# Performance work log

Hardware: AMD Instinct MI355X
Metric: run time of the kernel (lower is better)

The kernel has to match this reference:

```python
import jax, jax.numpy as jnp
import numpy as np


def _conv3d(x, w, b, strides):
    # x: (N, C, D, H, W), w: (O, I, kD, kH, kW), VALID padding like torch Conv3d p=0
    y = jax.lax.conv_general_dilated(
        x, w, window_strides=strides, padding='VALID',
        dimension_numbers=('NCDHW', 'OIDHW', 'NCDHW'))
    return y + b.reshape(1, -1, 1, 1, 1)


def _avgpool3d(x, k):
    y = jax.lax.reduce_window(x, 0.0, jax.lax.add,
                              (1, 1, k, k, k), (1, 1, k, k, k), 'VALID')
    return y / float(k ** 3)


def setup_inputs() -> dict:
    key = jax.random.key(0)
    ks = jax.random.split(key, 11)
    f = jnp.float32
    return {
        'x':  jax.random.normal(ks[0], (1, 10, 1, 52, 7, 24), dtype=f),
        'w1': jax.random.normal(ks[1], (1, 1, 6, 2, 2), dtype=f) * 0.2,
        'b1': jax.random.normal(ks[2], (1,), dtype=f) * 0.1,
        'w2': jax.random.normal(ks[3], (1, 1, 4, 1, 2), dtype=f) * 0.2,
        'b2': jax.random.normal(ks[4], (1,), dtype=f) * 0.1,
        'w4': jax.random.normal(ks[5], (80, 27), dtype=f) * 0.19,
        'b4': jax.random.normal(ks[6], (80,), dtype=f) * 0.1,
        'w5': jax.random.normal(ks[7], (200, 80), dtype=f) * 0.11,
        'b5': jax.random.normal(ks[8], (200,), dtype=f) * 0.1,
        'w6': jax.random.normal(ks[9], (676, 200), dtype=f) * 0.07,
        'b6': jax.random.normal(ks[10], (676,), dtype=f) * 0.1,
    }


def reference(x, w1, b1, w2, b2, w4, b4, w5, b5, w6, b6):
    xs = x[0]                                  # (10, 1, 52, 7, 24)
    weeks = xs.reshape(10, 52, 168)            # per-sample block used by trans()
    h = jax.nn.sigmoid(_conv3d(xs, w1, b1, (2, 1, 2)))   # (10, 1, 24, 6, 12)
    h = jax.nn.sigmoid(_conv3d(h, w2, b2, (4, 1, 2)))    # (10, 1, 6, 6, 6)
    h = _avgpool3d(h, 2)                                  # (10, 1, 3, 3, 3)
    h = h.reshape(10, 27)
    h = jax.nn.sigmoid(h @ w4.T + b4)
    h = jax.nn.sigmoid(h @ w5.T + b5)
    h = jax.nn.sigmoid(h @ w6.T + b6)          # (10, 676)
    # einsum('bj,bjk->bk', h, T) where T is block-diagonal: 13 identical
    # (52, 168) blocks of `weeks[b]` along the diagonal. Equivalent block form:
    out = jnp.einsum('bis,bsw->biw', h.reshape(10, 13, 52), weeks)
    return out.reshape(10, 13 * 168)           # (10, 2184)
```

## Files before the change

### kernel.cpp

```cpp
#include <hip/hip_runtime.h>
#include <math.h>


__device__ __forceinline__ float sigmoidf(float x) {
    return 1.0f / (1.0f + expf(-x));
}

__global__ __launch_bounds__(256) void c3dnet_fused(
    const float* __restrict__ x,
    const float* __restrict__ w1,
    const float* __restrict__ b1,
    const float* __restrict__ w2,
    const float* __restrict__ b2,
    const float* __restrict__ w4,
    const float* __restrict__ b4,
    const float* __restrict__ w5,
    const float* __restrict__ b5,
    const float* __restrict__ w6,
    const float* __restrict__ b6,
    float* __restrict__ out)
{
    const int b   = blockIdx.x;
    const int tid = threadIdx.x;

    __shared__ __align__(16) float xs_sh[8736];
    __shared__ __align__(16) float h1_sh[1728];
    __shared__ __align__(16) float h2_sh[216];
    __shared__ __align__(16) float pool_sh[27];
    __shared__ __align__(16) float f1_sh[80];
    __shared__ __align__(16) float f2_sh[200];
    __shared__ __align__(16) float f3_sh[676];
    __shared__ float w1_sh[24];
    __shared__ float w2_sh[8];
    __shared__ float b1_sh, b2_sh;

    {
        const float4* src = (const float4*)(x + (size_t)b * 8736);
        float4* dst = (float4*)xs_sh;
        for (int i = tid; i < 2184; i += 256) dst[i] = src[i];
        if (tid < 24) w1_sh[tid] = w1[tid];
        if (tid < 8)  w2_sh[tid] = w2[tid];
        if (tid == 0) { b1_sh = b1[0]; b2_sh = b2[0]; }
    }
    __syncthreads();

    for (int o = tid; o < 1728; o += 256) {
        const int d = o / 72;
        const int r = o % 72;
        const int h = r / 12;
        const int w = r % 12;
        const float* src = &xs_sh[(2 * d) * 168 + h * 24 + 2 * w];
        float acc = b1_sh;
        #pragma unroll
        for (int kd = 0; kd < 6; ++kd)
            #pragma unroll
            for (int kh = 0; kh < 2; ++kh)
                #pragma unroll
                for (int kw = 0; kw < 2; ++kw)
                    acc += src[kd * 168 + kh * 24 + kw] * w1_sh[kd * 4 + kh * 2 + kw];
        h1_sh[o] = sigmoidf(acc);
    }
    __syncthreads();

    if (tid < 216) {
        const int d = tid / 36;
        const int r = tid % 36;
        const int h = r / 6;
        const int w = r % 6;
        float acc = b2_sh;
        #pragma unroll
        for (int kd = 0; kd < 4; ++kd)
            #pragma unroll
            for (int kw = 0; kw < 2; ++kw)
                acc += h1_sh[(4 * d + kd) * 72 + h * 12 + (2 * w + kw)] * w2_sh[kd * 2 + kw];
        h2_sh[tid] = sigmoidf(acc);
    }
    __syncthreads();

    if (tid < 27) {
        const int d = tid / 9;
        const int r = tid % 9;
        const int h = r / 3;
        const int w = r % 3;
        float s = 0.f;
        #pragma unroll
        for (int dd = 0; dd < 2; ++dd)
            #pragma unroll
            for (int hh = 0; hh < 2; ++hh)
                #pragma unroll
                for (int ww = 0; ww < 2; ++ww)
                    s += h2_sh[(2 * d + dd) * 36 + (2 * h + hh) * 6 + (2 * w + ww)];
        pool_sh[tid] = s * 0.125f;
    }
    __syncthreads();

    if (tid < 80) {
        const float* wr = w4 + tid * 27;
        float acc = b4[tid];
        #pragma unroll
        for (int i = 0; i < 27; ++i) acc += pool_sh[i] * wr[i];
        f1_sh[tid] = sigmoidf(acc);
    }
    __syncthreads();

    if (tid < 200) {
        const float4* wr = (const float4*)(w5 + tid * 80);
        const float4* fv = (const float4*)f1_sh;
        float acc = b5[tid];
        #pragma unroll
        for (int i = 0; i < 20; ++i) {
            float4 a = wr[i], c = fv[i];
            acc += a.x * c.x + a.y * c.y + a.z * c.z + a.w * c.w;
        }
        f2_sh[tid] = sigmoidf(acc);
    }
    __syncthreads();

    for (int o = tid; o < 676; o += 256) {
        const float4* wr = (const float4*)(w6 + o * 200);
        const float4* fv = (const float4*)f2_sh;
        float acc = b6[o];
        #pragma unroll 10
        for (int i = 0; i < 50; ++i) {
            float4 a = wr[i], c = fv[i];
            acc += a.x * c.x + a.y * c.y + a.z * c.z + a.w * c.w;
        }
        f3_sh[o] = sigmoidf(acc);
    }
    __syncthreads();

    float* ob = out + (size_t)b * 2184;
    for (int o = tid; o < 2184; o += 256) {
        const int i = o / 168;
        const int w = o % 168;
        const float* fr = &f3_sh[i * 52];
        float acc = 0.f;
        #pragma unroll 13
        for (int s = 0; s < 52; ++s)
            acc += fr[s] * xs_sh[s * 168 + w];
        ob[o] = acc;
    }
}

extern "C" void kernel_launch(void* const* d_in, const int* in_sizes, int n_in,
                              void* d_out, int out_size, void* d_ws, size_t ws_size,
                              hipStream_t stream) {
    const float* x  = (const float*)d_in[0];
    const float* w1 = (const float*)d_in[1];
    const float* b1 = (const float*)d_in[2];
    const float* w2 = (const float*)d_in[3];
    const float* b2 = (const float*)d_in[4];
    const float* w4 = (const float*)d_in[5];
    const float* b4 = (const float*)d_in[6];
    const float* w5 = (const float*)d_in[7];
    const float* b5 = (const float*)d_in[8];
    const float* w6 = (const float*)d_in[9];
    const float* b6 = (const float*)d_in[10];
    float* out = (float*)d_out;

    c3dnet_fused<<<10, 256, 0, stream>>>(x, w1, b1, w2, b2, w4, b4,
                                         w5, b5, w6, b6, out);
}
```

Measured before the change: 94.89 us.

## Split fused network across 13x10 grid, vectorize conv1 and output einsum

```diff
diff --git a/kernel.cpp b/kernel.cpp
--- a/kernel.cpp
+++ b/kernel.cpp
@@ -3,7 +3,7 @@
 
 
 __device__ __forceinline__ float sigmoidf(float x) {
-    return 1.0f / (1.0f + expf(-x));
+    return 1.0f / (1.0f + __expf(-x));
 }
 
 __global__ __launch_bounds__(256) void c3dnet_fused(
@@ -20,7 +20,8 @@
     const float* __restrict__ b6,
     float* __restrict__ out)
 {
-    const int b   = blockIdx.x;
+    const int i0  = blockIdx.x;
+    const int b   = blockIdx.y;
     const int tid = threadIdx.x;
 
     __shared__ __align__(16) float xs_sh[8736];
@@ -29,36 +30,37 @@
     __shared__ __align__(16) float pool_sh[27];
     __shared__ __align__(16) float f1_sh[80];
     __shared__ __align__(16) float f2_sh[200];
-    __shared__ __align__(16) float f3_sh[676];
-    __shared__ float w1_sh[24];
-    __shared__ float w2_sh[8];
-    __shared__ float b1_sh, b2_sh;
+    __shared__ __align__(16) float f3_sh[52];
 
     {
         const float4* src = (const float4*)(x + (size_t)b * 8736);
         float4* dst = (float4*)xs_sh;
         for (int i = tid; i < 2184; i += 256) dst[i] = src[i];
-        if (tid < 24) w1_sh[tid] = w1[tid];
-        if (tid < 8)  w2_sh[tid] = w2[tid];
-        if (tid == 0) { b1_sh = b1[0]; b2_sh = b2[0]; }
     }
     __syncthreads();
 
-    for (int o = tid; o < 1728; o += 256) {
-        const int d = o / 72;
-        const int r = o % 72;
-        const int h = r / 12;
-        const int w = r % 12;
-        const float* src = &xs_sh[(2 * d) * 168 + h * 24 + 2 * w];
-        float acc = b1_sh;
-        #pragma unroll
-        for (int kd = 0; kd < 6; ++kd)
+    {
+        const float4* xs4 = (const float4*)xs_sh;
+        for (int t = tid; t < 864; t += 256) {
+            const int d = t / 36;
+            const int r = t % 36;
+            const int h = r / 6;
+            const int j = r % 6;
+            const int base4 = 84 * d + 6 * h + j;
+            float acc0 = b1[0], acc1 = b1[0];
             #pragma unroll
-            for (int kh = 0; kh < 2; ++kh)
+            for (int kd = 0; kd < 6; ++kd)
                 #pragma unroll
-                for (int kw = 0; kw < 2; ++kw)
-                    acc += src[kd * 168 + kh * 24 + kw] * w1_sh[kd * 4 + kh * 2 + kw];
-        h1_sh[o] = sigmoidf(acc);
+                for (int kh = 0; kh < 2; ++kh) {
+                    float4 v = xs4[base4 + kd * 42 + kh * 6];
+                    const float wk0 = w1[kd * 4 + kh * 2];
+                    const float wk1 = w1[kd * 4 + kh * 2 + 1];
+                    acc0 += v.x * wk0 + v.y * wk1;
+                    acc1 += v.z * wk0 + v.w * wk1;
+                }
+            h1_sh[d * 72 + h * 12 + 2 * j]     = sigmoidf(acc0);
+            h1_sh[d * 72 + h * 12 + 2 * j + 1] = sigmoidf(acc1);
+        }
     }
     __syncthreads();
 
@@ -67,12 +69,12 @@
         const int r = tid % 36;
         const int h = r / 6;
         const int w = r % 6;
-        float acc = b2_sh;
+        float acc = b2[0];
         #pragma unroll
         for (int kd = 0; kd < 4; ++kd)
             #pragma unroll
             for (int kw = 0; kw < 2; ++kw)
-                acc += h1_sh[(4 * d + kd) * 72 + h * 12 + (2 * w + kw)] * w2_sh[kd * 2 + kw];
+                acc += h1_sh[(4 * d + kd) * 72 + h * 12 + (2 * w + kw)] * w2[kd * 2 + kw];
         h2_sh[tid] = sigmoidf(acc);
     }
     __syncthreads();
@@ -116,29 +118,34 @@
     }
     __syncthreads();
 
-    for (int o = tid; o < 676; o += 256) {
-        const float4* wr = (const float4*)(w6 + o * 200);
+    if (tid < 52) {
+        const int row = i0 * 52 + tid;
+        const float4* wr = (const float4*)(w6 + row * 200);
         const float4* fv = (const float4*)f2_sh;
-        float acc = b6[o];
+        float acc = b6[row];
         #pragma unroll 10
         for (int i = 0; i < 50; ++i) {
             float4 a = wr[i], c = fv[i];
             acc += a.x * c.x + a.y * c.y + a.z * c.z + a.w * c.w;
         }
-        f3_sh[o] = sigmoidf(acc);
+        f3_sh[tid] = sigmoidf(acc);
     }
     __syncthreads();
 
-    float* ob = out + (size_t)b * 2184;
-    for (int o = tid; o < 2184; o += 256) {
-        const int i = o / 168;
-        const int w = o % 168;
-        const float* fr = &f3_sh[i * 52];
-        float acc = 0.f;
+    if (tid < 42) {
+        const float4* xs4 = (const float4*)xs_sh;
+        float4 acc = make_float4(0.f, 0.f, 0.f, 0.f);
         #pragma unroll 13
-        for (int s = 0; s < 52; ++s)
-            acc += fr[s] * xs_sh[s * 168 + w];
-        ob[o] = acc;
+        for (int s = 0; s < 52; ++s) {
+            const float fs = f3_sh[s];
+            float4 v = xs4[s * 42 + tid];
+            acc.x += fs * v.x;
+            acc.y += fs * v.y;
+            acc.z += fs * v.z;
+            acc.w += fs * v.w;
+        }
+        float4* ob = (float4*)(out + (size_t)b * 2184 + i0 * 168);
+        ob[tid] = acc;
     }
 }
 
@@ -158,6 +165,7 @@
     const float* b6 = (const float*)d_in[10];
     float* out = (float*)d_out;
 
-    c3dnet_fused<<<10, 256, 0, stream>>>(x, w1, b1, w2, b2, w4, b4,
-                                         w5, b5, w6, b6, out);
+    dim3 grid(13, 10);
+    c3dnet_fused<<<grid, 256, 0, stream>>>(x, w1, b1, w2, b2, w4, b4,
+                                           w5, b5, w6, b6, out);
 }
```

Measured after the change: 83.09 us. 1.14x faster.
